# Kernel tuning notes

Hardware: AMD Instinct MI355X
Metric: run time of the kernel (lower is better)

Reference implementation:

```python
import jax, jax.numpy as jnp
import numpy as np

L, H, E, HS, T, B, V = 6, 12, 768, 64, 1024, 2, 32000
EPS = 1e-5


def layer_norm(x, g, b):
    mu = jnp.mean(x, axis=-1, keepdims=True)
    var = jnp.mean(jnp.square(x - mu), axis=-1, keepdims=True)
    return (x - mu) * jax.lax.rsqrt(var + EPS) * g + b


def setup_inputs() -> dict:
    key = jax.random.key(0)
    ks = jax.random.split(key, 24)
    s = 0.02
    inp = {
        "idx": jax.random.randint(ks[0], (B, T), 0, V),
        "targets": jax.random.randint(ks[1], (B, T), 0, V),
        "tok_emb": jax.random.normal(ks[2], (V, E), jnp.float32) * s,
        "pos_emb": jax.random.normal(ks[3], (T, E), jnp.float32) * s,
        "ln1_g": jnp.ones((L, E), jnp.float32),
        "ln1_b": jnp.zeros((L, E), jnp.float32),
        "wq": jax.random.normal(ks[4], (L, E, E), jnp.float32) * s,
        "wk": jax.random.normal(ks[5], (L, E, E), jnp.float32) * s,
        "wv": jax.random.normal(ks[6], (L, E, E), jnp.float32) * s,
        "wproj": jax.random.normal(ks[7], (L, E, E), jnp.float32) * s,
        "bproj": jnp.zeros((L, E), jnp.float32),
        "ln2_g": jnp.ones((L, E), jnp.float32),
        "ln2_b": jnp.zeros((L, E), jnp.float32),
        "w1": jax.random.normal(ks[8], (L, E, 4 * E), jnp.float32) * s,
        "b1": jnp.zeros((L, 4 * E), jnp.float32),
        "w2": jax.random.normal(ks[9], (L, 4 * E, E), jnp.float32) * s,
        "b2": jnp.zeros((L, E), jnp.float32),
        "lnf_g": jnp.ones((E,), jnp.float32),
        "lnf_b": jnp.zeros((E,), jnp.float32),
        "lm_w": jax.random.normal(ks[10], (E, V), jnp.float32) * s,
        "lm_b": jnp.zeros((V,), jnp.float32),
    }
    return inp


def reference(idx, targets, tok_emb, pos_emb, ln1_g, ln1_b, wq, wk, wv, wproj,
              bproj, ln2_g, ln2_b, w1, b1, w2, b2, lnf_g, lnf_b, lm_w, lm_b):
    x = tok_emb[idx] + pos_emb[None, :T, :]  # [B,T,E]
    causal = jnp.tril(jnp.ones((T, T), bool))
    scale = E ** (-0.5)  # NOTE: original scales by n_embed**-0.5, not head_size
    for l in range(L):
        h = layer_norm(x, ln1_g[l], ln1_b[l])
        q = (h @ wq[l]).reshape(B, T, H, HS)
        k = (h @ wk[l]).reshape(B, T, H, HS)
        v = (h @ wv[l]).reshape(B, T, H, HS)
        scores = jnp.einsum('bqhd,bkhd->bhqk', q, k) * scale
        scores = jnp.where(causal[None, None], scores, -jnp.inf)
        w = jax.nn.softmax(scores, axis=-1)
        attn = jnp.einsum('bhqk,bkhd->bqhd', w, v).reshape(B, T, E)
        # original MultiHeadAttention applies proj TWICE (faithful reproduction)
        out = attn @ wproj[l] + bproj[l]
        out = out @ wproj[l] + bproj[l]
        x = x + out
        h2 = layer_norm(x, ln2_g[l], ln2_b[l])
        x = x + (jax.nn.relu(h2 @ w1[l] + b1[l]) @ w2[l] + b2[l])
    x = layer_norm(x, lnf_g, lnf_b)
    logits = x @ lm_w + lm_b  # [B,T,V]
    logp = jax.nn.log_softmax(logits, axis=-1)
    nll = -jnp.take_along_axis(logp, targets[..., None], axis=-1)[..., 0]
    loss = jnp.mean(nll)
    return logits, loss
```

## Files before the change

kernel.cpp:

```cpp
#include <hip/hip_runtime.h>
#include <math.h>

#define NL 6
#define NH 12
#define NE 768
#define NHS 64
#define NT 1024
#define NB 2
#define NV 32000
#define NM (NB * NT)
#define NQKV (3 * NE)
#define NFF (4 * NE)
#define LN_EPS 1e-5f

typedef __attribute__((ext_vector_type(8))) short short8;
typedef __attribute__((ext_vector_type(4))) float f32x4;
typedef __attribute__((ext_vector_type(4))) unsigned short ushort4v;
typedef __attribute__((address_space(1))) const unsigned int as1_cuint;
typedef __attribute__((address_space(3))) unsigned int as3_uint;

__device__ __forceinline__ unsigned short f2bf(float f) {
    unsigned int u = __builtin_bit_cast(unsigned int, f);
    u += 0x7fffu + ((u >> 16) & 1u);
    return (unsigned short)(u >> 16);
}
__device__ __forceinline__ float bf2f(unsigned short u) {
    unsigned int v = ((unsigned int)u) << 16;
    return __builtin_bit_cast(float, v);
}
__device__ __forceinline__ void gload_lds16(const void* g, void* l) {
    __builtin_amdgcn_global_load_lds((as1_cuint*)g, (as3_uint*)l, 16, 0, 0);
}

__global__ __launch_bounds__(256) void embed_ln_kernel(const int* __restrict__ idx,
                                                       const float* __restrict__ tok,
                                                       const float* __restrict__ pos,
                                                       const float* __restrict__ g,
                                                       const float* __restrict__ b,
                                                       float* __restrict__ x,
                                                       unsigned short* __restrict__ hbuf) {
    __shared__ float red[256];
    int row = blockIdx.x, tid = threadIdx.x;
    int t = row % NT;
    int id = idx[row];
    float v[3]; float s = 0.f;
    #pragma unroll
    for (int k = 0; k < 3; ++k) {
        int c = tid + k * 256;
        v[k] = tok[(long)id * NE + c] + pos[(long)t * NE + c];
        x[(long)row * NE + c] = v[k];
        s += v[k];
    }
    red[tid] = s; __syncthreads();
    for (int o = 128; o > 0; o >>= 1) { if (tid < o) red[tid] += red[tid + o]; __syncthreads(); }
    float mu = red[0] / NE;
    __syncthreads();
    float vr = 0.f;
    #pragma unroll
    for (int k = 0; k < 3; ++k) { float d = v[k] - mu; vr += d * d; }
    red[tid] = vr; __syncthreads();
    for (int o = 128; o > 0; o >>= 1) { if (tid < o) red[tid] += red[tid + o]; __syncthreads(); }
    float rstd = rsqrtf(red[0] / NE + LN_EPS);
    #pragma unroll
    for (int k = 0; k < 3; ++k) {
        int c = tid + k * 256;
        hbuf[(long)row * NE + c] = f2bf((v[k] - mu) * rstd * g[c] + b[c]);
    }
}

template<int S>
__global__ __launch_bounds__(256) void combine_ln_kernel(const float* __restrict__ parts,
                                                         const float* __restrict__ bias,
                                                         float* __restrict__ x,
                                                         const float* __restrict__ g,
                                                         const float* __restrict__ b,
                                                         unsigned short* __restrict__ hbuf) {
    __shared__ float red[256];
    int row = blockIdx.x, tid = threadIdx.x;
    float v[3]; float s = 0.f;
    #pragma unroll
    for (int k = 0; k < 3; ++k) {
        int c = tid + k * 256;
        long i = (long)row * NE + c;
        float a = parts[i];
        #pragma unroll
        for (int si = 1; si < S; ++si) a += parts[(long)si * NM * NE + i];
        a += bias[c] + x[i];
        x[i] = a;
        v[k] = a; s += a;
    }
    red[tid] = s; __syncthreads();
    for (int o = 128; o > 0; o >>= 1) { if (tid < o) red[tid] += red[tid + o]; __syncthreads(); }
    float mu = red[0] / NE;
    __syncthreads();
    float vr = 0.f;
    #pragma unroll
    for (int k = 0; k < 3; ++k) { float d = v[k] - mu; vr += d * d; }
    red[tid] = vr; __syncthreads();
    for (int o = 128; o > 0; o >>= 1) { if (tid < o) red[tid] += red[tid + o]; __syncthreads(); }
    float rstd = rsqrtf(red[0] / NE + LN_EPS);
    #pragma unroll
    for (int k = 0; k < 3; ++k) {
        int c = tid + k * 256;
        hbuf[(long)row * NE + c] = f2bf((v[k] - mu) * rstd * g[c] + b[c]);
    }
}

__global__ __launch_bounds__(256) void transpose4b_kernel(const float* __restrict__ wq,
                                                          const float* __restrict__ wk,
                                                          const float* __restrict__ wv,
                                                          const float* __restrict__ wp,
                                                          unsigned short* __restrict__ wqkvT,
                                                          unsigned short* __restrict__ wprojT) {
    __shared__ float t[32][33];
    int z = blockIdx.z, l = z >> 2, which = z & 3;
    const float* W = ((which == 0) ? wq : (which == 1) ? wk : (which == 2) ? wv : wp) + (long)l * NE * NE;
    unsigned short* WT = (which < 3) ? (wqkvT + (long)l * NQKV * NE + (long)which * NE * NE)
                                     : (wprojT + (long)l * NE * NE);
    int k0 = blockIdx.y * 32, n0 = blockIdx.x * 32;
    int c = threadIdx.x & 31, r = threadIdx.x >> 5;
    #pragma unroll
    for (int p = 0; p < 4; ++p)
        t[r + p * 8][c] = W[(long)(k0 + r + p * 8) * NE + n0 + c];
    __syncthreads();
    #pragma unroll
    for (int p = 0; p < 4; ++p)
        WT[(long)(n0 + r + p * 8) * NE + k0 + c] = f2bf(t[c][r + p * 8]);
}

__global__ __launch_bounds__(256) void transpose_cast_b_kernel(const float* __restrict__ W0,
                                                               unsigned short* __restrict__ WT0,
                                                               int K, int N) {
    __shared__ float t[32][33];
    long lofs = (long)blockIdx.z * K * N;
    const float* W = W0 + lofs;
    unsigned short* WT = WT0 + lofs;
    int k0 = blockIdx.y * 32, n0 = blockIdx.x * 32;
    int c = threadIdx.x & 31, r = threadIdx.x >> 5;
    #pragma unroll
    for (int p = 0; p < 4; ++p)
        t[r + p * 8][c] = W[(long)(k0 + r + p * 8) * N + n0 + c];
    __syncthreads();
    #pragma unroll
    for (int p = 0; p < 4; ++p)
        WT[(long)(n0 + r + p * 8) * K + k0 + c] = f2bf(t[c][r + p * 8]);
}

__global__ __launch_bounds__(256) void cast_kernel(const float* __restrict__ W,
                                                   unsigned short* __restrict__ O, long n) {
    long i = ((long)blockIdx.x * 256 + threadIdx.x) * 4;
    if (i < n) {
        float4 v = *(const float4*)(W + i);
        ushort4v o;
        o[0] = f2bf(v.x); o[1] = f2bf(v.y); o[2] = f2bf(v.z); o[3] = f2bf(v.w);
        *(ushort4v*)(O + i) = o;
    }
}

__global__ __launch_bounds__(256) void beff_b_kernel(const float* __restrict__ bproj,
                                                     const unsigned short* __restrict__ wprojT,
                                                     float* __restrict__ beff) {
    __shared__ float red[256];
    int n = blockIdx.x, l = blockIdx.y, tid = threadIdx.x;
    const unsigned short* wp = wprojT + (long)l * NE * NE + (long)n * NE;
    const float* bp = bproj + (long)l * NE;
    float acc = 0.f;
    for (int j = tid; j < NE; j += 256) acc += bp[j] * bf2f(wp[j]);
    red[tid] = acc; __syncthreads();
    for (int o = 128; o > 0; o >>= 1) { if (tid < o) red[tid] += red[tid + o]; __syncthreads(); }
    if (tid == 0) beff[(long)l * NE + n] = red[0] + bp[n];
}

template<typename OutT, bool BIAS, bool RELU, int SPLITK>
__global__ __launch_bounds__(256) void gemm_mfma(const unsigned short* __restrict__ A,
                                                 const unsigned short* __restrict__ BT,
                                                 const float* __restrict__ bias,
                                                 OutT* __restrict__ C,
                                                 int gridM, int N, int K) {
    __shared__ unsigned short As[3][128 * 32];
    __shared__ unsigned short Bs[3][128 * 32];
    int tid = threadIdx.x;
    int lane = tid & 63, w = tid >> 6;
    int wr = w >> 1, wc = w & 1;
    int l4 = lane >> 4, l15 = lane & 15;

    int nwg = gridDim.x, orig = blockIdx.x;
    int q = nwg >> 3, r8 = nwg & 7;
    int xcd = orig & 7, ii = orig >> 3;
    int wg = (xcd < r8) ? (xcd * (q + 1) + ii) : (r8 * (q + 1) + (xcd - r8) * q + ii);
    int bm = wg % gridM, bn = wg / gridM;
    int m0 = bm * 128, n0 = bn * 128;

    int kb = K / SPLITK;
    int koff = (SPLITK > 1) ? blockIdx.y * kb : 0;
    int nkt = kb >> 5;

    f32x4 acc[4][4] = {};

    int srow = lane >> 2;
    int scol = ((lane & 3) ^ ((lane >> 3) & 3)) * 8;
    int rsw  = (l4 ^ ((l15 >> 1) & 3)) * 8;

    auto STAGE = [&](int slot, int kt) {
        #pragma unroll
        for (int it = 0; it < 2; ++it) {
            int rr = w * 32 + it * 16;
            gload_lds16(&A [(long)(m0 + rr + srow) * K + koff + kt * 32 + scol], &As[slot][rr * 32]);
            gload_lds16(&BT[(long)(n0 + rr + srow) * K + koff + kt * 32 + scol], &Bs[slot][rr * 32]);
        }
    };

    STAGE(0, 0);
    if (nkt > 1) STAGE(1, 1);

    int s = 0;
    for (int t = 0; t < nkt; ++t) {
        if (t + 2 < nkt) STAGE((t + 2) % 3, t + 2);
        int ahead = nkt - 1 - t;
        if (ahead >= 2)      asm volatile("s_waitcnt vmcnt(8)" ::: "memory");
        else if (ahead == 1) asm volatile("s_waitcnt vmcnt(4)" ::: "memory");
        else                 asm volatile("s_waitcnt vmcnt(0)" ::: "memory");
        asm volatile("s_barrier" ::: "memory");

        short8 a[4], b[4];
        #pragma unroll
        for (int f = 0; f < 4; ++f) {
            a[f] = *(const short8*)&As[s][(wr * 64 + f * 16 + l15) * 32 + rsw];
            b[f] = *(const short8*)&Bs[s][(wc * 64 + f * 16 + l15) * 32 + rsw];
        }
        asm volatile("s_waitcnt lgkmcnt(0)" ::: "memory");
        asm volatile("s_barrier" ::: "memory");

        __builtin_amdgcn_s_setprio(1);
        #pragma unroll
        for (int fm = 0; fm < 4; ++fm)
            #pragma unroll
            for (int fn = 0; fn < 4; ++fn)
                acc[fm][fn] = __builtin_amdgcn_mfma_f32_16x16x32_bf16(a[fm], b[fn], acc[fm][fn], 0, 0, 0);
        __builtin_amdgcn_s_setprio(0);
        s = (s + 1) % 3;
    }

    if constexpr (SPLITK > 1) {
        float* Cp = (float*)C + (long)blockIdx.y * gridM * 128 * N;
        #pragma unroll
        for (int fm = 0; fm < 4; ++fm)
            #pragma unroll
            for (int j = 0; j < 4; ++j) {
                long row = m0 + wr * 64 + fm * 16 + l4 * 4 + j;
                #pragma unroll
                for (int fn = 0; fn < 4; ++fn)
                    Cp[row * N + n0 + wc * 64 + fn * 16 + l15] = acc[fm][fn][j];
            }
    } else {
        float bs[4];
        #pragma unroll
        for (int fn = 0; fn < 4; ++fn)
            bs[fn] = BIAS ? bias[n0 + wc * 64 + fn * 16 + l15] : 0.f;

        #pragma unroll
        for (int fm = 0; fm < 4; ++fm) {
            #pragma unroll
            for (int j = 0; j < 4; ++j) {
                long row = m0 + wr * 64 + fm * 16 + l4 * 4 + j;
                #pragma unroll
                for (int fn = 0; fn < 4; ++fn) {
                    int col = n0 + wc * 64 + fn * 16 + l15;
                    float v = acc[fm][fn][j] + bs[fn];
                    if (RELU) v = fmaxf(v, 0.f);
                    if constexpr (sizeof(OutT) == 2) C[row * N + col] = (OutT)f2bf(v);
                    else                             C[row * N + col] = v;
                }
            }
        }
    }
}

__global__ __launch_bounds__(256) void gemm_weff_kernel(const unsigned short* __restrict__ A0,
                                                        const unsigned short* __restrict__ B0,
                                                        unsigned short* __restrict__ C0,
                                                        int gridM, int N, int K) {
    __shared__ unsigned short As[2][128 * 32];
    __shared__ unsigned short Bs[2][128 * 32];
    long zofs = (long)blockIdx.z * N * K;
    const unsigned short* A = A0 + zofs;
    const unsigned short* BT = B0 + zofs;
    unsigned short* C = C0 + zofs;
    int tid = threadIdx.x;
    int lane = tid & 63, w = tid >> 6;
    int wr = w >> 1, wc = w & 1;
    int l4 = lane >> 4, l15 = lane & 15;
    int bm = blockIdx.x % gridM, bn = blockIdx.x / gridM;
    int m0 = bm * 128, n0 = bn * 128;

    f32x4 acc[4][4] = {};
    int srow = lane >> 2;
    int scol = ((lane & 3) ^ ((lane >> 3) & 3)) * 8;
    int rsw  = (l4 ^ ((l15 >> 1) & 3)) * 8;

    #pragma unroll
    for (int it = 0; it < 2; ++it) {
        int rr = w * 32 + it * 16;
        gload_lds16(&A [(long)(m0 + rr + srow) * K + scol], &As[0][rr * 32]);
        gload_lds16(&BT[(long)(n0 + rr + srow) * K + scol], &Bs[0][rr * 32]);
    }
    int cur = 0;
    for (int k0 = 0; k0 < K; k0 += 32) {
        __syncthreads();
        if (k0 + 32 < K) {
            #pragma unroll
            for (int it = 0; it < 2; ++it) {
                int rr = w * 32 + it * 16;
                gload_lds16(&A [(long)(m0 + rr + srow) * K + k0 + 32 + scol], &As[cur ^ 1][rr * 32]);
                gload_lds16(&BT[(long)(n0 + rr + srow) * K + k0 + 32 + scol], &Bs[cur ^ 1][rr * 32]);
            }
        }
        short8 a[4], b[4];
        #pragma unroll
        for (int f = 0; f < 4; ++f) {
            a[f] = *(const short8*)&As[cur][(wr * 64 + f * 16 + l15) * 32 + rsw];
            b[f] = *(const short8*)&Bs[cur][(wc * 64 + f * 16 + l15) * 32 + rsw];
        }
        #pragma unroll
        for (int fm = 0; fm < 4; ++fm)
            #pragma unroll
            for (int fn = 0; fn < 4; ++fn)
                acc[fm][fn] = __builtin_amdgcn_mfma_f32_16x16x32_bf16(a[fm], b[fn], acc[fm][fn], 0, 0, 0);
        cur ^= 1;
    }
    #pragma unroll
    for (int fm = 0; fm < 4; ++fm)
        #pragma unroll
        for (int j = 0; j < 4; ++j) {
            long row = m0 + wr * 64 + fm * 16 + l4 * 4 + j;
            #pragma unroll
            for (int fn = 0; fn < 4; ++fn)
                C[row * N + n0 + wc * 64 + fn * 16 + l15] = f2bf(acc[fm][fn][j]);
        }
}

__global__ __launch_bounds__(512, 4) void gemm256x128_lse(const unsigned short* __restrict__ A,
                                                          const unsigned short* __restrict__ BT,
                                                          const float* __restrict__ bias,
                                                          float* __restrict__ C,
                                                          float* __restrict__ pm, float* __restrict__ ps,
                                                          int gridM, int N, int K) {
    __shared__ unsigned short Al[3][256 * 32];
    __shared__ unsigned short Bl[3][128 * 32];
    int tid = threadIdx.x;
    int lane = tid & 63, w = tid >> 6;
    int wm = w >> 1, wn = w & 1;
    int l4 = lane >> 4, l15 = lane & 15;

    int nwg = gridDim.x, orig = blockIdx.x;
    int q = nwg >> 3, r8 = nwg & 7;
    int xcd = orig & 7, ii = orig >> 3;
    int wg = (xcd < r8) ? (xcd * (q + 1) + ii) : (r8 * (q + 1) + (xcd - r8) * q + ii);
    int bm = wg % gridM, bn = wg / gridM;
    int m0 = bm * 256, n0 = bn * 128;

    int nkt = K >> 5;
    int srow = lane >> 2;
    int sslot = ((lane & 3) ^ ((lane >> 3) & 3)) * 8;

    auto STAGE = [&](int slot, int kt) {
        #pragma unroll
        for (int p = 0; p < 2; ++p) {
            int r0 = p * 128 + w * 16;
            gload_lds16(&A[(long)(m0 + r0 + srow) * K + kt * 32 + sslot], &Al[slot][r0 * 32]);
        }
        int r0 = w * 16;
        gload_lds16(&BT[(long)(n0 + r0 + srow) * K + kt * 32 + sslot], &Bl[slot][r0 * 32]);
    };

    f32x4 acc[4][4] = {};
    int rsw = (l4 ^ ((l15 >> 1) & 3)) * 8;

    STAGE(0, 0);
    STAGE(1, 1);
    int s = 0;
    for (int t = 0; t < nkt; ++t) {
        if (t + 2 < nkt) STAGE((t + 2) % 3, t + 2);
        int ahead = nkt - 1 - t;
        if (ahead >= 2)      asm volatile("s_waitcnt vmcnt(6)" ::: "memory");
        else if (ahead == 1) asm volatile("s_waitcnt vmcnt(3)" ::: "memory");
        else                 asm volatile("s_waitcnt vmcnt(0)" ::: "memory");
        asm volatile("s_barrier" ::: "memory");

        short8 af[4], bf[4];
        #pragma unroll
        for (int f = 0; f < 4; ++f) {
            af[f] = *(const short8*)&Al[s][(wm * 64 + f * 16 + l15) * 32 + rsw];
            bf[f] = *(const short8*)&Bl[s][(wn * 64 + f * 16 + l15) * 32 + rsw];
        }
        asm volatile("s_waitcnt lgkmcnt(0)" ::: "memory");
        asm volatile("s_barrier" ::: "memory");

        __builtin_amdgcn_s_setprio(1);
        #pragma unroll
        for (int fm = 0; fm < 4; ++fm)
            #pragma unroll
            for (int fn = 0; fn < 4; ++fn)
                acc[fm][fn] = __builtin_amdgcn_mfma_f32_16x16x32_bf16(af[fm], bf[fn], acc[fm][fn], 0, 0, 0);
        __builtin_amdgcn_s_setprio(0);
        s = (s + 1) % 3;
    }

    float bs[4];
    #pragma unroll
    for (int fn = 0; fn < 4; ++fn)
        bs[fn] = bias[n0 + wn * 64 + fn * 16 + l15];

    #pragma unroll
    for (int fm = 0; fm < 4; ++fm) {
        #pragma unroll
        for (int j = 0; j < 4; ++j) {
            long row = m0 + wm * 64 + fm * 16 + l4 * 4 + j;
            float v4[4];
            #pragma unroll
            for (int fn = 0; fn < 4; ++fn) {
                int col = n0 + wn * 64 + fn * 16 + l15;
                float v = acc[fm][fn][j] + bs[fn];
                __builtin_nontemporal_store(v, &C[row * N + col]);
                v4[fn] = v;
            }
            float mx = fmaxf(fmaxf(v4[0], v4[1]), fmaxf(v4[2], v4[3]));
            #pragma unroll
            for (int off = 1; off < 16; off <<= 1) mx = fmaxf(mx, __shfl_xor(mx, off));
            float sm = 0.f;
            #pragma unroll
            for (int fn = 0; fn < 4; ++fn) sm += __expf(v4[fn] - mx);
            #pragma unroll
            for (int off = 1; off < 16; off <<= 1) sm += __shfl_xor(sm, off);
            if (l15 == 0) {
                int pidx = bn * 2 + wn;
                pm[row * 512 + pidx] = mx;
                ps[row * 512 + pidx] = sm;
            }
        }
    }
}

__global__ __launch_bounds__(256) void vtrans_kernel(const unsigned short* __restrict__ qkv,
                                                     unsigned short* __restrict__ vt) {
    __shared__ unsigned short t[64][72];
    int t0 = blockIdx.x * 64;
    int bh = blockIdx.y;
    int b = bh / NH, h = bh % NH;
    int tid = threadIdx.x;
    #pragma unroll
    for (int i = 0; i < 2; ++i) {
        int r = (tid >> 3) + i * 32, c8 = (tid & 7) * 8;
        short8 v = *(const short8*)(qkv + ((long)b * NT + t0 + r) * NQKV + 2 * NE + h * NHS + c8);
        *(short8*)&t[r][c8] = v;
    }
    __syncthreads();
    #pragma unroll
    for (int i = 0; i < 2; ++i) {
        int d = (tid >> 3) + i * 32, s = (tid & 7) * 8;
        short8 o;
        #pragma unroll
        for (int j = 0; j < 8; ++j) o[j] = (short)t[s + j][d];
        *(short8*)(vt + ((long)bh * NHS + d) * NT + t0 + s) = o;
    }
}

__global__ __launch_bounds__(512) void fattn_kernel(const unsigned short* __restrict__ qkv,
                                                    const unsigned short* __restrict__ vt,
                                                    unsigned short* __restrict__ out) {
    __shared__ unsigned short Ks[2][64 * 64];
    __shared__ unsigned short Vl[2][64 * 64];
    __shared__ unsigned short Ps[8 * 16 * 64];
    int qt = gridDim.x - 1 - blockIdx.x;
    int bh = blockIdx.y;
    int b = bh / NH, h = bh % NH;
    int tid = threadIdx.x, lane = tid & 63, w = tid >> 6;
    int l4 = lane >> 4, l15 = lane & 15;
    long rowb = (long)b * NT;
    const float scale = 0.03608439182435161f;
    const unsigned short* vtp = vt + (long)bh * NHS * NT;

    const unsigned short* qptr = qkv + (rowb + qt * 128 + w * 16 + l15) * NQKV + h * NHS;
    short8 qa0 = *(const short8*)(qptr + l4 * 8);
    short8 qa1 = *(const short8*)(qptr + 32 + l4 * 8);

    f32x4 o[4] = {};
    float m[4], lsum[4];
    #pragma unroll
    for (int j = 0; j < 4; ++j) { m[j] = -INFINITY; lsum[j] = 0.f; }

    int kr_r = tid >> 3, kr_c = (tid & 7) * 8;
    int vr_d = tid >> 3, vr_s = tid & 7;

    short8 kr, vr;
    auto LOADT = [&](int t) {
        int kbase = t * 64;
        kr = *(const short8*)(qkv + (rowb + kbase + kr_r) * NQKV + NE + h * NHS + kr_c);
        vr = *(const short8*)(vtp + (long)vr_d * NT + kbase + vr_s * 8);
    };

    int ntiles = 2 * qt + 2;
    LOADT(0);
    for (int t = 0; t < ntiles; ++t) {
        int cur = t & 1;
        *(short8*)&Ks[cur][kr_r * 64 + (kr_c ^ ((kr_r & 7) << 3))] = kr;
        *(short8*)&Vl[cur][vr_d * 64 + ((vr_s * 8) ^ ((vr_d & 7) << 3))] = vr;
        asm volatile("s_waitcnt lgkmcnt(0)" ::: "memory");
        if (t + 1 < ntiles) LOADT(t + 1);
        asm volatile("s_barrier" ::: "memory");

        f32x4 s[4];
        __builtin_amdgcn_s_setprio(1);
        #pragma unroll
        for (int fn = 0; fn < 4; ++fn) {
            int key = fn * 16 + l15;
            short8 kb0 = *(const short8*)&Ks[cur][key * 64 + ((l4 * 8) ^ ((key & 7) << 3))];
            short8 kb1 = *(const short8*)&Ks[cur][key * 64 + ((32 + l4 * 8) ^ ((key & 7) << 3))];
            f32x4 z = {};
            z = __builtin_amdgcn_mfma_f32_16x16x32_bf16(qa0, kb0, z, 0, 0, 0);
            s[fn] = __builtin_amdgcn_mfma_f32_16x16x32_bf16(qa1, kb1, z, 0, 0, 0);
        }
        __builtin_amdgcn_s_setprio(0);

        if (t >= 2 * qt) {
            #pragma unroll
            for (int fn = 0; fn < 4; ++fn) {
                int key = t * 64 + fn * 16 + l15;
                #pragma unroll
                for (int j = 0; j < 4; ++j) {
                    int qrow = qt * 128 + w * 16 + l4 * 4 + j;
                    s[fn][j] = (key <= qrow) ? s[fn][j] * scale : -1e30f;
                }
            }
        } else {
            #pragma unroll
            for (int fn = 0; fn < 4; ++fn)
                #pragma unroll
                for (int j = 0; j < 4; ++j)
                    s[fn][j] *= scale;
        }

        #pragma unroll
        for (int j = 0; j < 4; ++j) {
            float mj = fmaxf(fmaxf(s[0][j], s[1][j]), fmaxf(s[2][j], s[3][j]));
            #pragma unroll
            for (int off = 1; off < 16; off <<= 1) mj = fmaxf(mj, __shfl_xor(mj, off));
            float mnew = fmaxf(m[j], mj);
            float alpha = __expf(m[j] - mnew);
            m[j] = mnew;
            float psum = 0.f;
            #pragma unroll
            for (int fn = 0; fn < 4; ++fn) {
                float p = __expf(s[fn][j] - mnew);
                psum += p;
                int rr = l4 * 4 + j, c = fn * 16 + l15;
                Ps[w * 1024 + rr * 64 + (c ^ ((rr & 7) << 3))] = f2bf(p);
            }
            #pragma unroll
            for (int off = 1; off < 16; off <<= 1) psum += __shfl_xor(psum, off);
            lsum[j] = lsum[j] * alpha + psum;
            #pragma unroll
            for (int fn = 0; fn < 4; ++fn) o[fn][j] *= alpha;
        }

        short8 pa0 = *(const short8*)&Ps[w * 1024 + l15 * 64 + ((l4 * 8) ^ ((l15 & 7) << 3))];
        short8 pa1 = *(const short8*)&Ps[w * 1024 + l15 * 64 + ((32 + l4 * 8) ^ ((l15 & 7) << 3))];
        __builtin_amdgcn_s_setprio(1);
        #pragma unroll
        for (int fn = 0; fn < 4; ++fn) {
            int d = fn * 16 + l15;
            short8 vb0 = *(const short8*)&Vl[cur][d * 64 + ((l4 * 8) ^ ((d & 7) << 3))];
            short8 vb1 = *(const short8*)&Vl[cur][d * 64 + ((32 + l4 * 8) ^ ((d & 7) << 3))];
            o[fn] = __builtin_amdgcn_mfma_f32_16x16x32_bf16(pa0, vb0, o[fn], 0, 0, 0);
            o[fn] = __builtin_amdgcn_mfma_f32_16x16x32_bf16(pa1, vb1, o[fn], 0, 0, 0);
        }
        __builtin_amdgcn_s_setprio(0);
    }

    #pragma unroll
    for (int j = 0; j < 4; ++j) {
        long row = rowb + qt * 128 + w * 16 + l4 * 4 + j;
        float inv = 1.0f / lsum[j];
        #pragma unroll
        for (int fn = 0; fn < 4; ++fn)
            out[row * NE + h * NHS + fn * 16 + l15] = f2bf(o[fn][j] * inv);
    }
}

__global__ __launch_bounds__(256) void nll_combine_kernel(const float* __restrict__ logits,
                                                          const float* __restrict__ pm,
                                                          const float* __restrict__ ps,
                                                          const int* __restrict__ targets,
                                                          float* __restrict__ nll) {
    __shared__ float rm[256], rs[256];
    int row = blockIdx.x, tid = threadIdx.x;
    float m = -1e30f, s = 0.f;
    for (int i = tid; i < 500; i += 256) {
        float m2 = pm[(long)row * 512 + i], s2 = ps[(long)row * 512 + i];
        float mm = fmaxf(m, m2);
        s = s * __expf(m - mm) + s2 * __expf(m2 - mm);
        m = mm;
    }
    rm[tid] = m; rs[tid] = s; __syncthreads();
    for (int o = 128; o > 0; o >>= 1) {
        if (tid < o) {
            float m2 = rm[tid + o], s2 = rs[tid + o];
            float mm = fmaxf(rm[tid], m2);
            rs[tid] = rs[tid] * __expf(rm[tid] - mm) + s2 * __expf(m2 - mm);
            rm[tid] = mm;
        }
        __syncthreads();
    }
    if (tid == 0) {
        int tgt = targets[row];
        nll[row] = -(logits[(long)row * NV + tgt] - rm[0] - logf(rs[0]));
    }
}

__global__ void loss_reduce_kernel(const float* __restrict__ nll, float* __restrict__ out) {
    __shared__ float red[256];
    int tid = threadIdx.x;
    float s = 0.f;
    for (int i = tid; i < NM; i += 256) s += nll[i];
    red[tid] = s; __syncthreads();
    for (int o = 128; o > 0; o >>= 1) { if (tid < o) red[tid] += red[tid + o]; __syncthreads(); }
    if (tid == 0) out[0] = red[0] / NM;
}

extern "C" void kernel_launch(void* const* d_in, const int* in_sizes, int n_in,
                              void* d_out, int out_size, void* d_ws, size_t ws_size,
                              hipStream_t stream) {
    const int*   idx     = (const int*)  d_in[0];
    const int*   targets = (const int*)  d_in[1];
    const float* tok     = (const float*)d_in[2];
    const float* pos     = (const float*)d_in[3];
    const float* ln1_g   = (const float*)d_in[4];
    const float* ln1_b   = (const float*)d_in[5];
    const float* wq      = (const float*)d_in[6];
    const float* wk      = (const float*)d_in[7];
    const float* wv      = (const float*)d_in[8];
    const float* wproj   = (const float*)d_in[9];
    const float* bproj   = (const float*)d_in[10];
    const float* ln2_g   = (const float*)d_in[11];
    const float* ln2_b   = (const float*)d_in[12];
    const float* w1      = (const float*)d_in[13];
    const float* b1      = (const float*)d_in[14];
    const float* w2      = (const float*)d_in[15];
    const float* b2      = (const float*)d_in[16];
    const float* lnf_g   = (const float*)d_in[17];
    const float* lnf_b   = (const float*)d_in[18];
    const float* lm_w    = (const float*)d_in[19];
    const float* lm_b    = (const float*)d_in[20];

    float* logits = (float*)d_out;
    float* loss   = logits + (long)NM * NV;

    char* p = (char*)d_ws;
    float*          x      = (float*)p;          p += (long)NM * NE * 4;
    unsigned short* hbuf   = (unsigned short*)p; p += (long)NM * NE * 2;
    unsigned short* qkv    = (unsigned short*)p; p += (long)NM * NQKV * 2;
    unsigned short* att    = (unsigned short*)p; p += (long)NM * NE * 2;
    unsigned short* hid    = (unsigned short*)p; p += (long)NM * NFF * 2;
    unsigned short* vt     = (unsigned short*)p; p += (long)NB * NH * NHS * NT * 2;
    float*          nll    = (float*)p;          p += (long)NM * 4;
    float*          pmb    = (float*)p;          p += (long)NM * 512 * 4;
    float*          psb    = (float*)p;          p += (long)NM * 512 * 4;
    float*          parts  = (float*)p;          p += (long)2 * NM * NQKV * 4;
    unsigned short* wqkvT6 = (unsigned short*)p; p += (long)NL * NQKV * NE * 2;
    unsigned short* wprojT6= (unsigned short*)p; p += (long)NL * NE * NE * 2;
    unsigned short* wprojC6= (unsigned short*)p; p += (long)NL * NE * NE * 2;
    unsigned short* weffT6 = (unsigned short*)p; p += (long)NL * NE * NE * 2;
    float*          beff6  = (float*)p;          p += (long)NL * NE * 4;
    unsigned short* w1T6   = (unsigned short*)p; p += (long)NL * NFF * NE * 2;
    unsigned short* w2T6   = (unsigned short*)p; p += (long)NL * NE * NFF * 2;
    unsigned short* lmT    = (unsigned short*)p; p += (long)NV * NE * 2;

    dim3 blk(256);

    transpose4b_kernel<<<dim3(NE / 32, NE / 32, 4 * NL), blk, 0, stream>>>(
        wq, wk, wv, wproj, wqkvT6, wprojT6);
    cast_kernel<<<(NL * NE * NE) / 1024, blk, 0, stream>>>(wproj, wprojC6, (long)NL * NE * NE);
    transpose_cast_b_kernel<<<dim3(NFF / 32, NE / 32, NL), blk, 0, stream>>>(w1, w1T6, NE, NFF);
    transpose_cast_b_kernel<<<dim3(NE / 32, NFF / 32, NL), blk, 0, stream>>>(w2, w2T6, NFF, NE);
    gemm_weff_kernel<<<dim3(36, 1, NL), blk, 0, stream>>>(wprojT6, wprojC6, weffT6, 6, NE, NE);
    beff_b_kernel<<<dim3(NE, NL), blk, 0, stream>>>(bproj, wprojT6, beff6);
    transpose_cast_b_kernel<<<dim3(NV / 32, NE / 32, 1), blk, 0, stream>>>(lm_w, lmT, NE, NV);

    embed_ln_kernel<<<NM, blk, 0, stream>>>(idx, tok, pos, ln1_g, ln1_b, x, hbuf);

    for (int l = 0; l < NL; ++l) {
        gemm_mfma<unsigned short, false, false, 1><<<dim3((NM/128)*(NQKV/128)), blk, 0, stream>>>(
            hbuf, wqkvT6 + (long)l * NQKV * NE, nullptr, qkv, NM / 128, NQKV, NE);
        vtrans_kernel<<<dim3(NT / 64, NB * NH), blk, 0, stream>>>(qkv, vt);
        fattn_kernel<<<dim3(NT / 128, NB * NH), dim3(512), 0, stream>>>(qkv, vt, att);
        gemm_mfma<float, false, false, 2><<<dim3((NM/128)*(NE/128), 2), blk, 0, stream>>>(
            att, weffT6 + (long)l * NE * NE, nullptr, parts, NM / 128, NE, NE);
        combine_ln_kernel<2><<<NM, blk, 0, stream>>>(
            parts, beff6 + (long)l * NE, x, ln2_g + (long)l * NE, ln2_b + (long)l * NE, hbuf);
        gemm_mfma<unsigned short, true, true, 1><<<dim3((NM/128)*(NFF/128)), blk, 0, stream>>>(
            hbuf, w1T6 + (long)l * NFF * NE, b1 + (long)l * NFF, hid, NM / 128, NFF, NE);
        gemm_mfma<float, false, false, 4><<<dim3((NM/128)*(NE/128), 4), blk, 0, stream>>>(
            hid, w2T6 + (long)l * NE * NFF, nullptr, parts, NM / 128, NE, NFF);
        const float* ng = (l < NL - 1) ? (ln1_g + (long)(l + 1) * NE) : lnf_g;
        const float* nb = (l < NL - 1) ? (ln1_b + (long)(l + 1) * NE) : lnf_b;
        combine_ln_kernel<4><<<NM, blk, 0, stream>>>(parts, b2 + (long)l * NE, x, ng, nb, hbuf);
    }

    gemm256x128_lse<<<dim3((NM/256)*(NV/128)), dim3(512), 0, stream>>>(
        hbuf, lmT, lm_b, logits, pmb, psb, NM / 256, NV, NE);
    nll_combine_kernel<<<NM, blk, 0, stream>>>(logits, pmb, psb, targets, nll);
    loss_reduce_kernel<<<1, blk, 0, stream>>>(nll, loss);
}
```

Baseline: 1.087 ms.

## Use BK=64 double buffering in LM-head GEMM and per-wave softmax max in attention

The LM-head GEMM with fused log-sum-exp moves from a 3-stage pipeline with 32-wide K tiles to a 2-stage pipeline with 64-wide K tiles and a new XOR swizzle. This halves the number of barrier rounds and doubles the MFMA work per round, but halves the occupancy hint and doubles LDS use per stage. Separately, the attention kernel now keeps a single wave-wide running max instead of per-row maxima. It rescales only when the max rises and defers the row-sum shuffle reduction to the end, cutting per-tile shuffles and exps at some risk to numerical range if rows differ widely.

```diff
diff --git a/kernel.cpp b/kernel.cpp
--- a/kernel.cpp
+++ b/kernel.cpp
@@ -339,14 +339,14 @@
         }
 }
 
-__global__ __launch_bounds__(512, 4) void gemm256x128_lse(const unsigned short* __restrict__ A,
+__global__ __launch_bounds__(512, 2) void gemm256x128_lse(const unsigned short* __restrict__ A,
                                                           const unsigned short* __restrict__ BT,
                                                           const float* __restrict__ bias,
                                                           float* __restrict__ C,
                                                           float* __restrict__ pm, float* __restrict__ ps,
                                                           int gridM, int N, int K) {
-    __shared__ unsigned short Al[3][256 * 32];
-    __shared__ unsigned short Bl[3][128 * 32];
+    __shared__ unsigned short Al[2][256 * 64];
+    __shared__ unsigned short Bl[2][128 * 64];
     int tid = threadIdx.x;
     int lane = tid & 63, w = tid >> 6;
     int wm = w >> 1, wn = w & 1;
@@ -359,51 +359,60 @@
     int bm = wg % gridM, bn = wg / gridM;
     int m0 = bm * 256, n0 = bn * 128;
 
-    int nkt = K >> 5;
-    int srow = lane >> 2;
-    int sslot = ((lane & 3) ^ ((lane >> 3) & 3)) * 8;
+    int nkt = K >> 6;
+    int lr = lane >> 3, lc = lane & 7;
 
     auto STAGE = [&](int slot, int kt) {
         #pragma unroll
-        for (int p = 0; p < 2; ++p) {
-            int r0 = p * 128 + w * 16;
-            gload_lds16(&A[(long)(m0 + r0 + srow) * K + kt * 32 + sslot], &Al[slot][r0 * 32]);
-        }
-        int r0 = w * 16;
-        gload_lds16(&BT[(long)(n0 + r0 + srow) * K + kt * 32 + sslot], &Bl[slot][r0 * 32]);
+        for (int i = 0; i < 4; ++i) {
+            int row = (w * 4 + i) * 8 + lr;
+            gload_lds16(&A[(long)(m0 + row) * K + kt * 64 + (lc ^ (row & 7)) * 8],
+                        &Al[slot][(w * 4 + i) * 8 * 64]);
+        }
+        #pragma unroll
+        for (int i = 0; i < 2; ++i) {
+            int row = (w * 2 + i) * 8 + lr;
+            gload_lds16(&BT[(long)(n0 + row) * K + kt * 64 + (lc ^ (row & 7)) * 8],
+                        &Bl[slot][(w * 2 + i) * 8 * 64]);
+        }
     };
 
     f32x4 acc[4][4] = {};
-    int rsw = (l4 ^ ((l15 >> 1) & 3)) * 8;
 
     STAGE(0, 0);
-    STAGE(1, 1);
-    int s = 0;
     for (int t = 0; t < nkt; ++t) {
-        if (t + 2 < nkt) STAGE((t + 2) % 3, t + 2);
-        int ahead = nkt - 1 - t;
-        if (ahead >= 2)      asm volatile("s_waitcnt vmcnt(6)" ::: "memory");
-        else if (ahead == 1) asm volatile("s_waitcnt vmcnt(3)" ::: "memory");
-        else                 asm volatile("s_waitcnt vmcnt(0)" ::: "memory");
+        if (t + 1 < nkt) {
+            STAGE((t + 1) & 1, t + 1);
+            asm volatile("s_waitcnt vmcnt(6)" ::: "memory");
+        } else {
+            asm volatile("s_waitcnt vmcnt(0)" ::: "memory");
+        }
         asm volatile("s_barrier" ::: "memory");
 
-        short8 af[4], bf[4];
+        int s = t & 1;
+        short8 af[4][2], bf[4][2];
         #pragma unroll
         for (int f = 0; f < 4; ++f) {
-            af[f] = *(const short8*)&Al[s][(wm * 64 + f * 16 + l15) * 32 + rsw];
-            bf[f] = *(const short8*)&Bl[s][(wn * 64 + f * 16 + l15) * 32 + rsw];
+            int ra = wm * 64 + f * 16 + l15;
+            int rb = wn * 64 + f * 16 + l15;
+            #pragma unroll
+            for (int kk = 0; kk < 2; ++kk) {
+                af[f][kk] = *(const short8*)&Al[s][ra * 64 + ((kk * 4 + l4) ^ (ra & 7)) * 8];
+                bf[f][kk] = *(const short8*)&Bl[s][rb * 64 + ((kk * 4 + l4) ^ (rb & 7)) * 8];
+            }
         }
         asm volatile("s_waitcnt lgkmcnt(0)" ::: "memory");
         asm volatile("s_barrier" ::: "memory");
 
         __builtin_amdgcn_s_setprio(1);
         #pragma unroll
-        for (int fm = 0; fm < 4; ++fm)
-            #pragma unroll
-            for (int fn = 0; fn < 4; ++fn)
-                acc[fm][fn] = __builtin_amdgcn_mfma_f32_16x16x32_bf16(af[fm], bf[fn], acc[fm][fn], 0, 0, 0);
+        for (int kk = 0; kk < 2; ++kk)
+            #pragma unroll
+            for (int fm = 0; fm < 4; ++fm)
+                #pragma unroll
+                for (int fn = 0; fn < 4; ++fn)
+                    acc[fm][fn] = __builtin_amdgcn_mfma_f32_16x16x32_bf16(af[fm][kk], bf[fn][kk], acc[fm][fn], 0, 0, 0);
         __builtin_amdgcn_s_setprio(0);
-        s = (s + 1) % 3;
     }
 
     float bs[4];
@@ -485,9 +494,8 @@
     short8 qa1 = *(const short8*)(qptr + 32 + l4 * 8);
 
     f32x4 o[4] = {};
-    float m[4], lsum[4];
-    #pragma unroll
-    for (int j = 0; j < 4; ++j) { m[j] = -INFINITY; lsum[j] = 0.f; }
+    float m = -INFINITY;
+    float lsum[4] = {};
 
     int kr_r = tid >> 3, kr_c = (tid & 7) * 8;
     int vr_d = tid >> 3, vr_s = tid & 7;
@@ -540,27 +548,37 @@
                     s[fn][j] *= scale;
         }
 
+        float tmax = -INFINITY;
+        #pragma unroll
+        for (int fn = 0; fn < 4; ++fn)
+            #pragma unroll
+            for (int j = 0; j < 4; ++j)
+                tmax = fmaxf(tmax, s[fn][j]);
+        #pragma unroll
+        for (int off = 1; off < 64; off <<= 1) tmax = fmaxf(tmax, __shfl_xor(tmax, off));
+
+        if (tmax > m) {
+            float alpha = __expf(m - tmax);
+            m = tmax;
+            #pragma unroll
+            for (int j = 0; j < 4; ++j) lsum[j] *= alpha;
+            #pragma unroll
+            for (int fn = 0; fn < 4; ++fn)
+                #pragma unroll
+                for (int j = 0; j < 4; ++j) o[fn][j] *= alpha;
+        }
+
         #pragma unroll
         for (int j = 0; j < 4; ++j) {
-            float mj = fmaxf(fmaxf(s[0][j], s[1][j]), fmaxf(s[2][j], s[3][j]));
-            #pragma unroll
-            for (int off = 1; off < 16; off <<= 1) mj = fmaxf(mj, __shfl_xor(mj, off));
-            float mnew = fmaxf(m[j], mj);
-            float alpha = __expf(m[j] - mnew);
-            m[j] = mnew;
             float psum = 0.f;
             #pragma unroll
             for (int fn = 0; fn < 4; ++fn) {
-                float p = __expf(s[fn][j] - mnew);
+                float p = __expf(s[fn][j] - m);
                 psum += p;
                 int rr = l4 * 4 + j, c = fn * 16 + l15;
                 Ps[w * 1024 + rr * 64 + (c ^ ((rr & 7) << 3))] = f2bf(p);
             }
-            #pragma unroll
-            for (int off = 1; off < 16; off <<= 1) psum += __shfl_xor(psum, off);
-            lsum[j] = lsum[j] * alpha + psum;
-            #pragma unroll
-            for (int fn = 0; fn < 4; ++fn) o[fn][j] *= alpha;
+            lsum[j] += psum;
         }
 
         short8 pa0 = *(const short8*)&Ps[w * 1024 + l15 * 64 + ((l4 * 8) ^ ((l15 & 7) << 3))];
@@ -576,6 +594,12 @@
         }
         __builtin_amdgcn_s_setprio(0);
     }
+
+    #pragma unroll
+    for (int j = 0; j < 4; ++j)
+        #pragma unroll
+        for (int off = 1; off < 16; off <<= 1)
+            lsum[j] += __shfl_xor(lsum[j], off);
 
     #pragma unroll
     for (int j = 0; j < 4; ++j) {
```

Measured after the change: 1.083 ms. About the same (-0.4%).
